# Performance work log

Hardware: AMD Instinct MI355X
Metric: run time of the kernel (lower is better)

## Reference

```python
import jax, jax.numpy as jnp
import numpy as np

D_IN, D_OUT, HEADS, D_K = 256, 256, 8, 32
B, N, L = 2, 128, 512
SCALING = 1.0 / np.sqrt(D_K)


def setup_inputs() -> dict:
    key = jax.random.key(0)
    ks = jax.random.split(key, 12)
    s = 0.02
    return {
        "query": jax.random.normal(ks[0], (B, L, D_IN), jnp.float32),
        "key": jax.random.normal(ks[1], (B, L, D_IN), jnp.float32),
        "value": jax.random.normal(ks[2], (B, N, L, D_OUT), jnp.float32),
        "mask": jax.random.uniform(ks[3], (B, 1, L, L), jnp.float32),
        "Wq": jax.random.normal(ks[4], (D_IN, HEADS * D_K), jnp.float32) * s,
        "bq": jnp.zeros((HEADS * D_K,), jnp.float32),
        "Wk": jax.random.normal(ks[5], (D_IN, HEADS * D_K), jnp.float32) * s,
        "bk": jnp.zeros((HEADS * D_K,), jnp.float32),
        "Wv": jax.random.normal(ks[6], (D_OUT, D_OUT), jnp.float32) * s,
        "bv": jnp.zeros((D_OUT,), jnp.float32),
        "Wo": jax.random.normal(ks[7], (D_OUT, D_OUT), jnp.float32) * s,
        "bo": jnp.zeros((D_OUT,), jnp.float32),
    }


def reference(query, key, value, mask, Wq, bq, Wk, bk, Wv, bv, Wo, bo):
    b, n, l = value.shape[:3]
    h, dk = HEADS, D_K
    dh = value.shape[-1] // h  # per-head value dim
    # projections -> per-head layouts
    q = (query @ Wq + bq).reshape(b, l, h, dk).transpose(0, 2, 1, 3)  # bhld
    k = (key @ Wk + bk).reshape(b, l, h, dk).transpose(0, 2, 1, 3)    # bhld
    v = (value @ Wv + bv).reshape(b, n, l, h, dh).transpose(0, 3, 1, 2, 4)  # bhnld
    q = q * SCALING
    scores = jnp.einsum('bhid,bhjd->bhij', q, k)  # (B,H,L,L)
    scores = jnp.where(mask < 0.5, jnp.finfo(scores.dtype).min, scores)
    attn = jax.nn.softmax(scores, axis=-1)
    # dropout omitted (eval mode / deterministic reference)
    out = jnp.einsum('bhij,bhnjd->bhnid', attn, v)  # (B,H,N,L,dh)
    out = out.transpose(0, 2, 3, 1, 4).reshape(b, n, l, h * dh)
    return out @ Wo + bo
```

## Files before the change

### kernel.cpp

```cpp
#include <hip/hip_runtime.h>
#include <hip/hip_bf16.h>
#include <stdint.h>

#define BB 2
#define LL 512
#define DIN 256
#define HH 8
#define DKK 32
#define NN 128
#define DM 256
#define SCALING 0.17677669529663687f

typedef unsigned short u16;
typedef float f32x4 __attribute__((ext_vector_type(4)));
typedef short s16x8 __attribute__((ext_vector_type(8)));

#define MFMA16(a, b, c) __builtin_amdgcn_mfma_f32_16x16x32_bf16((a), (b), (c), 0, 0, 0)

typedef __attribute__((address_space(3))) char lds_char;
typedef const __attribute__((address_space(1))) char glb_char;

__device__ __forceinline__ void gload16(const void* g, void* l) {
    __builtin_amdgcn_global_load_lds((glb_char*)g, (lds_char*)l, 16, 0, 0);
}

__device__ __forceinline__ u16 f2bf(float f) {
    union { float f; uint32_t i; } v; v.f = f;
    uint32_t x = v.i;
    return (u16)((x + 0x7fffu + ((x >> 16) & 1u)) >> 16);
}

__device__ __forceinline__ uint32_t pack2bf(float f0, float f1) {
    union { float f; uint32_t i; } a, b;
    a.f = f0; b.f = f1;
    return __builtin_amdgcn_perm(b.i + 0x8000u, a.i + 0x8000u, 0x07060302u);
}

__device__ __forceinline__ s16x8 ldsfrag(const u16* base, int row, int cb) {
    const char* p = (const char*)base + row * 128 + (cb ^ ((row & 7) << 4));
    return *(const s16x8*)(const void*)p;
}

__global__ __launch_bounds__(256) void prep_weights(
        const float* __restrict__ Wq, const float* __restrict__ Wk,
        const float* __restrict__ Wv, const float* __restrict__ Wo,
        u16* __restrict__ wqt, u16* __restrict__ wkt,
        u16* __restrict__ wvt, u16* __restrict__ wot) {
    int idx = blockIdx.x * 256 + threadIdx.x;
    int which = idx >> 16;
    const float* src = (which == 0) ? Wq : (which == 1) ? Wk : (which == 2) ? Wv : Wo;
    u16* dst = (which == 0) ? wqt : (which == 1) ? wkt : (which == 2) ? wvt : wot;
    int i = idx & 65535;
    int c = i & 255;
    int k = i >> 8;
    dst[(size_t)c * 256 + k] = f2bf(src[(size_t)k * 256 + c]);
}

__global__ __launch_bounds__(256) void qk_proj(
        const float* __restrict__ q_in, const float* __restrict__ k_in,
        const u16* __restrict__ wqt, const float* __restrict__ bq,
        const u16* __restrict__ wkt, const float* __restrict__ bk,
        u16* __restrict__ q_ws, u16* __restrict__ k_ws) {
    int bid = blockIdx.x;
    int isK = bid & 1;
    int r0 = (bid >> 1) * 64;
    const float* src = isK ? k_in : q_in;
    const u16* wt    = isK ? wkt : wqt;
    const float* bias = isK ? bk : bq;
    u16* dst = isK ? k_ws : q_ws;
    float scale = isK ? 1.0f : SCALING;

    int t = threadIdx.x, w = t >> 6, l = t & 63, lr = l & 15, lg = l >> 4;

    f32x4 zero = {0.f, 0.f, 0.f, 0.f};
    f32x4 acc[4][4];
#pragma unroll
    for (int m = 0; m < 4; m++)
#pragma unroll
        for (int cf = 0; cf < 4; cf++) acc[m][cf] = zero;

#pragma unroll
    for (int ks = 0; ks < 8; ks++) {
        s16x8 afr[4];
#pragma unroll
        for (int m = 0; m < 4; m++) {
            const float* p = src + (size_t)(r0 + m * 16 + lr) * DIN + ks * 32 + lg * 8;
            float4 v0 = *(const float4*)p;
            float4 v1 = *(const float4*)(p + 4);
            union { u16 u[8]; s16x8 v; } tmp;
            tmp.u[0] = f2bf(v0.x); tmp.u[1] = f2bf(v0.y);
            tmp.u[2] = f2bf(v0.z); tmp.u[3] = f2bf(v0.w);
            tmp.u[4] = f2bf(v1.x); tmp.u[5] = f2bf(v1.y);
            tmp.u[6] = f2bf(v1.z); tmp.u[7] = f2bf(v1.w);
            afr[m] = tmp.v;
        }
        s16x8 bfrg[4];
#pragma unroll
        for (int cf = 0; cf < 4; cf++)
            bfrg[cf] = *(const s16x8*)(const void*)(wt + (size_t)(w * 64 + cf * 16 + lr) * 256 + ks * 32 + lg * 8);
#pragma unroll
        for (int m = 0; m < 4; m++)
#pragma unroll
            for (int cf = 0; cf < 4; cf++) acc[m][cf] = MFMA16(afr[m], bfrg[cf], acc[m][cf]);
    }

#pragma unroll
    for (int m = 0; m < 4; m++)
#pragma unroll
        for (int cf = 0; cf < 4; cf++) {
            int c = w * 64 + cf * 16 + lr;
            int h = c >> 5, dd = c & 31;
            float bv_ = bias[c];
#pragma unroll
            for (int r = 0; r < 4; r++) {
                int row = r0 + m * 16 + 4 * lg + r;
                int b = row >> 9, li = row & 511;
                dst[(((size_t)(b * HH + h)) * LL + li) * DKK + dd] = f2bf((acc[m][cf][r] + bv_) * scale);
            }
        }
}

__global__ __launch_bounds__(256) void scores_softmax(
        const u16* __restrict__ q_ws, const u16* __restrict__ k_ws,
        const float* __restrict__ mask, u16* __restrict__ attn) {
    int bid = blockIdx.x;
    int it = bid & 15;
    int bh = bid >> 4;
    int b = bh >> 3;
    int i0 = it * 32;

    __shared__ u16 kl[LL][40];
    __shared__ u16 ql[32][40];
    __shared__ float redmx[2][32];
    __shared__ float redsm[2][32];

    int t = threadIdx.x;
    const u16* kbase = k_ws + (size_t)bh * LL * DKK;
#pragma unroll
    for (int x = 0; x < 8; x++) {
        int idx = x * 256 + t;
        int row = idx >> 2, ch = idx & 3;
        *(s16x8*)(void*)(&kl[row][ch * 8]) = *(const s16x8*)(const void*)(kbase + (size_t)row * DKK + ch * 8);
    }
    if (t < 128) {
        const u16* qbase = q_ws + (size_t)bh * LL * DKK + (size_t)i0 * DKK;
        int row = t >> 2, ch = t & 3;
        *(s16x8*)(void*)(&ql[row][ch * 8]) = *(const s16x8*)(const void*)(qbase + (size_t)row * DKK + ch * 8);
    }
    __syncthreads();

    int w = t >> 6, l = t & 63, lr = l & 15, lg = l >> 4;
    int ih = (w & 1) * 16;
    int jh = (w >> 1) * 256;
    int jhalf = w >> 1;

    s16x8 af = *(const s16x8*)(const void*)(&ql[ih + lr][lg * 8]);
    f32x4 zero = {0.f, 0.f, 0.f, 0.f};
    f32x4 acc[16];
#pragma unroll
    for (int cf = 0; cf < 16; cf++) {
        s16x8 bf = *(const s16x8*)(const void*)(&kl[jh + cf * 16 + lr][lg * 8]);
        acc[cf] = MFMA16(af, bf, zero);
    }

    const float* mrow = mask + (size_t)b * LL * LL;
    float attv[16][4];
    float mx[4], sm[4];
#pragma unroll
    for (int r = 0; r < 4; r++) mx[r] = -3.0e38f;
#pragma unroll
    for (int cf = 0; cf < 16; cf++) {
#pragma unroll
        for (int r = 0; r < 4; r++) {
            int irow = i0 + ih + 4 * lg + r;
            int jcol = jh + cf * 16 + lr;
            float mv = mrow[(size_t)irow * LL + jcol];
            float s = (mv < 0.5f) ? -1.0e30f : acc[cf][r];
            attv[cf][r] = s;
            mx[r] = fmaxf(mx[r], s);
        }
    }
#pragma unroll
    for (int d = 1; d < 16; d <<= 1)
#pragma unroll
        for (int r = 0; r < 4; r++) mx[r] = fmaxf(mx[r], __shfl_xor(mx[r], d));
#pragma unroll
    for (int r = 0; r < 4; r++) sm[r] = 0.f;
#pragma unroll
    for (int cf = 0; cf < 16; cf++)
#pragma unroll
        for (int r = 0; r < 4; r++) {
            float p = __expf(attv[cf][r] - mx[r]);
            attv[cf][r] = p;
            sm[r] += p;
        }
#pragma unroll
    for (int d = 1; d < 16; d <<= 1)
#pragma unroll
        for (int r = 0; r < 4; r++) sm[r] += __shfl_xor(sm[r], d);

    if (lr == 0) {
#pragma unroll
        for (int r = 0; r < 4; r++) {
            redmx[jhalf][ih + 4 * lg + r] = mx[r];
            redsm[jhalf][ih + 4 * lg + r] = sm[r];
        }
    }
    __syncthreads();
    float inv[4];
#pragma unroll
    for (int r = 0; r < 4; r++) {
        int row = ih + 4 * lg + r;
        float m0 = redmx[0][row], m1 = redmx[1][row];
        float s0 = redsm[0][row], s1 = redsm[1][row];
        float gm = fmaxf(m0, m1);
        float gs = s0 * __expf(m0 - gm) + s1 * __expf(m1 - gm);
        inv[r] = __expf(mx[r] - gm) / gs;
    }

    u16* abase = attn + (size_t)bh * LL * LL;
#pragma unroll
    for (int cf = 0; cf < 16; cf++)
#pragma unroll
        for (int r = 0; r < 4; r++) {
            int irow = i0 + ih + 4 * lg + r;
            int jcol = jh + cf * 16 + lr;
            abase[(size_t)irow * LL + jcol] = f2bf(attv[cf][r] * inv[r]);
        }
}

__global__ __launch_bounds__(256, 2) void vproj_gemm(
        const float* __restrict__ value, const float* __restrict__ bv,
        const u16* __restrict__ wvt, u16* __restrict__ ut) {
    __shared__ __align__(16) u16 sm[2 * 16384];

    int t = threadIdx.x;
    int nb = gridDim.x;
    int cpx = nb >> 3;
    int swz = (blockIdx.x & 7) * cpx + (blockIdx.x >> 3);
    int ct = swz & 1;
    int jt = (swz >> 1) & 3;
    int bn = swz >> 3;
    int c0 = ct * 128, j0 = jt * 128;

    int w = t >> 6, l = t & 63, lr = l & 15, lg = l >> 4;
    int wr = w >> 1, wc = w & 1;

    const float* vbase = value + ((size_t)bn * LL + j0) * DM;

    int srow = t >> 3;
    int sgc = t & 7;
    f32x4 zero = {0.f, 0.f, 0.f, 0.f};
    f32x4 acc[4][4];
#pragma unroll
    for (int m = 0; m < 4; m++)
#pragma unroll
        for (int nf = 0; nf < 4; nf++) acc[m][nf] = zero;

    auto stageA = [&](int buf, int kk) {
#pragma unroll
        for (int x = 0; x < 4; x++) {
            int row = x * 32 + srow;
            int gs = sgc ^ (row & 7);
            gload16(wvt + (size_t)(c0 + row) * 256 + kk * 64 + gs * 8,
                    (char*)&sm[buf * 16384] + (x * 256 + t) * 16);
        }
    };
    float4 breg[2][4][2];
    auto loadB = [&](int set, int kk) {
#pragma unroll
        for (int x = 0; x < 4; x++) {
            int row = x * 32 + srow;
            const float* p = vbase + (size_t)row * DM + kk * 64 + sgc * 8;
            breg[set][x][0] = *(const float4*)p;
            breg[set][x][1] = *(const float4*)(p + 4);
        }
    };
    auto writeB = [&](int buf, int set) {
#pragma unroll
        for (int x = 0; x < 4; x++) {
            int row = x * 32 + srow;
            uint32_t p0 = pack2bf(breg[set][x][0].x, breg[set][x][0].y);
            uint32_t p1 = pack2bf(breg[set][x][0].z, breg[set][x][0].w);
            uint32_t p2 = pack2bf(breg[set][x][1].x, breg[set][x][1].y);
            uint32_t p3 = pack2bf(breg[set][x][1].z, breg[set][x][1].w);
            uint32_t* dst = (uint32_t*)((char*)&sm[buf * 16384 + 8192]
                            + row * 128 + ((sgc * 16) ^ ((row & 7) << 4)));
            dst[0] = p0; dst[1] = p1; dst[2] = p2; dst[3] = p3;
        }
    };

    stageA(0, 0);
    loadB(0, 0);
    loadB(1, 1);
    writeB(0, 0);
    __syncthreads();
    int cur = 0;
#pragma unroll
    for (int kk = 0; kk < 4; kk++) {
        if (kk < 3) stageA(cur ^ 1, kk + 1);
        if (kk < 2) loadB(kk & 1, kk + 2);
        const u16* Ab = &sm[cur * 16384];
        const u16* Bb = &sm[cur * 16384 + 8192];
        s16x8 af[4][2], bf[4][2];
#pragma unroll
        for (int m = 0; m < 4; m++)
#pragma unroll
            for (int ks = 0; ks < 2; ks++)
                af[m][ks] = ldsfrag(Ab, wr * 64 + m * 16 + lr, ks * 64 + lg * 16);
#pragma unroll
        for (int nf = 0; nf < 4; nf++)
#pragma unroll
            for (int ks = 0; ks < 2; ks++)
                bf[nf][ks] = ldsfrag(Bb, wc * 64 + nf * 16 + lr, ks * 64 + lg * 16);
#pragma unroll
        for (int ks = 0; ks < 2; ks++)
#pragma unroll
            for (int m = 0; m < 4; m++)
#pragma unroll
                for (int nf = 0; nf < 4; nf++)
                    acc[m][nf] = MFMA16(af[m][ks], bf[nf][ks], acc[m][nf]);
        if (kk < 3) writeB(cur ^ 1, (kk + 1) & 1);
        __syncthreads();
        cur ^= 1;
    }

    u16* ubase = ut + (size_t)bn * DM * LL;
#pragma unroll
    for (int m = 0; m < 4; m++) {
#pragma unroll
        for (int rr = 0; rr < 4; rr++) {
            int c = c0 + wr * 64 + m * 16 + 4 * lg + rr;
            float bvv = bv[c];
#pragma unroll
            for (int nf = 0; nf < 4; nf++) {
                int j = j0 + wc * 64 + nf * 16 + lr;
                ubase[(size_t)c * LL + j] = f2bf(acc[m][nf][rr] + bvv);
            }
        }
    }
}

__global__ __launch_bounds__(256, 2) void pv_gemm(
        const u16* __restrict__ attn, const u16* __restrict__ ut,
        u16* __restrict__ Tm, int n0, int nTiles, int Nc) {
    __shared__ __align__(16) u16 sm[2 * 16384];

    int t = threadIdx.x;
    int nb = gridDim.x;
    int cpx = nb >> 3;
    int swz = (blockIdx.x & 7) * cpx + (blockIdx.x >> 3);
    int nct = swz % nTiles;
    int tmp2 = swz / nTiles;
    int it = tmp2 & 3;
    int bh = tmp2 >> 2;
    int b = bh >> 3, h = bh & 7;
    int i0 = it * 128;

    int w = t >> 6, l = t & 63, lr = l & 15, lg = l >> 4;
    int wr = w >> 1, wc = w & 1;

    const u16* arow0 = attn + (size_t)bh * LL * LL + (size_t)i0 * LL;

    f32x4 zero = {0.f, 0.f, 0.f, 0.f};
    f32x4 acc[4][4];
#pragma unroll
    for (int m = 0; m < 4; m++)
#pragma unroll
        for (int nf = 0; nf < 4; nf++) acc[m][nf] = zero;

    auto stage = [&](int buf, int kk) {
#pragma unroll
        for (int x = 0; x < 4; x++) {
            int G = x * 256 + t;
            int row = G >> 3, gc = G & 7;
            int gs = gc ^ (row & 7);
            gload16(arow0 + (size_t)row * LL + kk * 64 + gs * 8,
                    (char*)&sm[buf * 16384] + G * 16);
        }
#pragma unroll
        for (int x = 0; x < 4; x++) {
            int G = x * 256 + t;
            int row = G >> 3, gc = G & 7;
            int gs = gc ^ (row & 7);
            int nc = nct * 128 + row;
            const u16* src = ut + (((size_t)(b * NN + n0 + (nc >> 5))) * DM + h * DKK + (nc & 31)) * LL
                             + kk * 64 + gs * 8;
            gload16(src, (char*)&sm[buf * 16384 + 8192] + G * 16);
        }
    };

    stage(0, 0);
    __syncthreads();
    int cur = 0;
    for (int kk = 0; kk < 8; kk++) {
        if (kk < 7) stage(cur ^ 1, kk + 1);
        const u16* Ab = &sm[cur * 16384];
        const u16* Bb = &sm[cur * 16384 + 8192];
        s16x8 af[4][2], bf[4][2];
#pragma unroll
        for (int m = 0; m < 4; m++)
#pragma unroll
            for (int ks = 0; ks < 2; ks++)
                af[m][ks] = ldsfrag(Ab, wr * 64 + m * 16 + lr, ks * 64 + lg * 16);
#pragma unroll
        for (int nf = 0; nf < 4; nf++)
#pragma unroll
            for (int ks = 0; ks < 2; ks++)
                bf[nf][ks] = ldsfrag(Bb, wc * 64 + nf * 16 + lr, ks * 64 + lg * 16);
#pragma unroll
        for (int ks = 0; ks < 2; ks++)
#pragma unroll
            for (int m = 0; m < 4; m++)
#pragma unroll
                for (int nf = 0; nf < 4; nf++)
                    acc[m][nf] = MFMA16(af[m][ks], bf[nf][ks], acc[m][nf]);
        __syncthreads();
        cur ^= 1;
    }

#pragma unroll
    for (int m = 0; m < 4; m++) {
        int i = i0 + wr * 64 + m * 16 + 4 * lg;
#pragma unroll
        for (int nf = 0; nf < 4; nf++) {
            int nc = nct * 128 + wc * 64 + nf * 16 + lr;
            int nl = nc >> 5, cl = nc & 31;
            u16* dst = Tm + (((size_t)(b * Nc + nl)) * LL + i) * DM + h * DKK + cl;
#pragma unroll
            for (int rr = 0; rr < 4; rr++)
                dst[(size_t)rr * DM] = f2bf(acc[m][nf][rr]);
        }
    }
}

__global__ __launch_bounds__(256, 2) void wo_gemm(
        const u16* __restrict__ Tm, const u16* __restrict__ wot,
        const float* __restrict__ bo, float* __restrict__ out,
        int n0, int Nc, int nshift) {
    __shared__ __align__(16) u16 sm[2 * 16384];

    int t = threadIdx.x;
    int nb = gridDim.x;
    int cpx = nb >> 3;
    int swz = (blockIdx.x & 7) * cpx + (blockIdx.x >> 3);
    int oc = swz & 1;
    int mt = swz >> 1;
    int r0 = mt * 128;

    int w = t >> 6, l = t & 63, lr = l & 15, lg = l >> 4;
    int wr = w >> 1, wc = w & 1;

    f32x4 zero = {0.f, 0.f, 0.f, 0.f};
    f32x4 acc[4][4];
#pragma unroll
    for (int m = 0; m < 4; m++)
#pragma unroll
        for (int nf = 0; nf < 4; nf++) acc[m][nf] = zero;

    auto stage = [&](int buf, int kk) {
#pragma unroll
        for (int x = 0; x < 4; x++) {
            int G = x * 256 + t;
            int row = G >> 3, gc = G & 7;
            int gs = gc ^ (row & 7);
            gload16(Tm + (size_t)(r0 + row) * DM + kk * 64 + gs * 8,
                    (char*)&sm[buf * 16384] + G * 16);
        }
#pragma unroll
        for (int x = 0; x < 4; x++) {
            int G = x * 256 + t;
            int row = G >> 3, gc = G & 7;
            int gs = gc ^ (row & 7);
            gload16(wot + (size_t)(oc * 128 + row) * DM + kk * 64 + gs * 8,
                    (char*)&sm[buf * 16384 + 8192] + G * 16);
        }
    };

    stage(0, 0);
    __syncthreads();
    int cur = 0;
    for (int kk = 0; kk < 4; kk++) {
        if (kk < 3) stage(cur ^ 1, kk + 1);
        const u16* Ab = &sm[cur * 16384];
        const u16* Bb = &sm[cur * 16384 + 8192];
        s16x8 af[4][2], bf[4][2];
#pragma unroll
        for (int m = 0; m < 4; m++)
#pragma unroll
            for (int ks = 0; ks < 2; ks++)
                af[m][ks] = ldsfrag(Ab, wr * 64 + m * 16 + lr, ks * 64 + lg * 16);
#pragma unroll
        for (int nf = 0; nf < 4; nf++)
#pragma unroll
            for (int ks = 0; ks < 2; ks++)
                bf[nf][ks] = ldsfrag(Bb, wc * 64 + nf * 16 + lr, ks * 64 + lg * 16);
#pragma unroll
        for (int ks = 0; ks < 2; ks++)
#pragma unroll
            for (int m = 0; m < 4; m++)
#pragma unroll
                for (int nf = 0; nf < 4; nf++)
                    acc[m][nf] = MFMA16(af[m][ks], bf[nf][ks], acc[m][nf]);
        __syncthreads();
        cur ^= 1;
    }

#pragma unroll
    for (int nf = 0; nf < 4; nf++) {
        int ocol = oc * 128 + wc * 64 + nf * 16 + lr;
        float bov = bo[ocol];
#pragma unroll
        for (int m = 0; m < 4; m++) {
            int rbase = r0 + wr * 64 + m * 16 + 4 * lg;
#pragma unroll
            for (int rr = 0; rr < 4; rr++) {
                int r = rbase + rr;
                int bnl = r >> 9, i = r & 511;
                int b = bnl >> nshift, nl = bnl & (Nc - 1);
                out[(((size_t)(b * NN + n0 + nl)) * LL + i) * DM + ocol] = acc[m][nf][rr] + bov;
            }
        }
    }
}

extern "C" void kernel_launch(void* const* d_in, const int* in_sizes, int n_in,
                              void* d_out, int out_size, void* d_ws, size_t ws_size,
                              hipStream_t stream) {
    const float* query = (const float*)d_in[0];
    const float* key_  = (const float*)d_in[1];
    const float* value = (const float*)d_in[2];
    const float* mask  = (const float*)d_in[3];
    const float* Wq = (const float*)d_in[4];
    const float* bq = (const float*)d_in[5];
    const float* Wk = (const float*)d_in[6];
    const float* bk = (const float*)d_in[7];
    const float* Wv = (const float*)d_in[8];
    const float* bv = (const float*)d_in[9];
    const float* Wo = (const float*)d_in[10];
    const float* bo = (const float*)d_in[11];

    char* ws = (char*)d_ws;
    u16* wvt  = (u16*)(ws + 0);
    u16* wot  = (u16*)(ws + 131072);
    u16* qw   = (u16*)(ws + 262144);
    u16* kw   = (u16*)(ws + 786432);
    u16* attn = (u16*)(ws + 1310720);
    u16* wqt  = (u16*)(ws + 1310720);
    u16* wkt  = (u16*)(ws + 1310720 + 131072);
    u16* ut   = (u16*)(ws + 9699328);
    u16* Tm   = (u16*)(ws + 76808192);
    float* out = (float*)d_out;

    size_t avail = (ws_size > 76808192u) ? (ws_size - 76808192u) : 0;
    int Nc = 128;
    while (Nc > 4 && (size_t)Nc * 524288u > avail) Nc >>= 1;
    int nshift = 0;
    while ((1 << nshift) < Nc) nshift++;

    hipLaunchKernelGGL(prep_weights,   dim3(1024), dim3(256), 0, stream, Wq, Wk, Wv, Wo, wqt, wkt, wvt, wot);
    hipLaunchKernelGGL(qk_proj,        dim3(32),   dim3(256), 0, stream, query, key_, wqt, bq, wkt, bk, qw, kw);
    hipLaunchKernelGGL(scores_softmax, dim3(256),  dim3(256), 0, stream, qw, kw, mask, attn);
    hipLaunchKernelGGL(vproj_gemm,     dim3(2048), dim3(256), 0, stream, value, bv, wvt, ut);

    int nTiles = Nc >> 2;
    for (int n0 = 0; n0 < NN; n0 += Nc) {
        hipLaunchKernelGGL(pv_gemm, dim3(16 * 4 * nTiles), dim3(256), 0, stream,
                           attn, ut, Tm, n0, nTiles, Nc);
        hipLaunchKernelGGL(wo_gemm, dim3((BB * Nc * LL / 128) * 2), dim3(256), 0, stream,
                           Tm, wot, bo, out, n0, Nc, nshift);
    }
}
```

Before: 185.0 us.

## Make GEMM kernels persistent over multiple tiles with cross-tile prefetch

The V-projection, PV and Wo GEMM kernels now launch at most 512 blocks, and each block loops over several consecutive output tiles. The first k-slice of the next tile is staged into shared memory while the last k-slice of the current tile is being computed, so the pipeline does not drain between tiles. This aims to cut block launch and prologue costs and keep the loads flowing. In exchange there is less block-level parallelism, a longer serial chain per block, and the epilogue stores now sit inside the main loop.

```diff
diff --git a/kernel.cpp b/kernel.cpp
--- a/kernel.cpp
+++ b/kernel.cpp
@@ -231,25 +231,28 @@
 
 __global__ __launch_bounds__(256, 2) void vproj_gemm(
         const float* __restrict__ value, const float* __restrict__ bv,
-        const u16* __restrict__ wvt, u16* __restrict__ ut) {
+        const u16* __restrict__ wvt, u16* __restrict__ ut, int tpb) {
     __shared__ __align__(16) u16 sm[2 * 16384];
 
     int t = threadIdx.x;
     int nb = gridDim.x;
     int cpx = nb >> 3;
-    int swz = (blockIdx.x & 7) * cpx + (blockIdx.x >> 3);
-    int ct = swz & 1;
-    int jt = (swz >> 1) & 3;
-    int bn = swz >> 3;
-    int c0 = ct * 128, j0 = jt * 128;
+    int sb = (blockIdx.x & 7) * cpx + (blockIdx.x >> 3);
+    int g0 = sb * tpb;
 
     int w = t >> 6, l = t & 63, lr = l & 15, lg = l >> 4;
     int wr = w >> 1, wc = w & 1;
-
-    const float* vbase = value + ((size_t)bn * LL + j0) * DM;
-
     int srow = t >> 3;
     int sgc = t & 7;
+
+    int c0_c, j0_c, bn_c, c0_n, j0_n, bn_n;
+    const float *vb_c, *vb_n;
+    {
+        int ct = g0 & 1, jt = (g0 >> 1) & 3, bn = g0 >> 3;
+        c0_c = ct * 128; j0_c = jt * 128; bn_c = bn;
+        vb_c = value + ((size_t)bn * LL + j0_c) * DM;
+    }
+
     f32x4 zero = {0.f, 0.f, 0.f, 0.f};
     f32x4 acc[4][4];
 #pragma unroll
@@ -257,7 +260,7 @@
 #pragma unroll
         for (int nf = 0; nf < 4; nf++) acc[m][nf] = zero;
 
-    auto stageA = [&](int buf, int kk) {
+    auto stageA = [&](int buf, int c0, int kk) {
 #pragma unroll
         for (int x = 0; x < 4; x++) {
             int row = x * 32 + srow;
@@ -267,11 +270,11 @@
         }
     };
     float4 breg[2][4][2];
-    auto loadB = [&](int set, int kk) {
+    auto loadB = [&](int set, const float* vb, int kk) {
 #pragma unroll
         for (int x = 0; x < 4; x++) {
             int row = x * 32 + srow;
-            const float* p = vbase + (size_t)row * DM + kk * 64 + sgc * 8;
+            const float* p = vb + (size_t)row * DM + kk * 64 + sgc * 8;
             breg[set][x][0] = *(const float4*)p;
             breg[set][x][1] = *(const float4*)(p + 4);
         }
@@ -290,77 +293,100 @@
         }
     };
 
-    stageA(0, 0);
-    loadB(0, 0);
-    loadB(1, 1);
+    stageA(0, c0_c, 0);
+    loadB(0, vb_c, 0);
+    loadB(1, vb_c, 1);
     writeB(0, 0);
     __syncthreads();
     int cur = 0;
-#pragma unroll
-    for (int kk = 0; kk < 4; kk++) {
-        if (kk < 3) stageA(cur ^ 1, kk + 1);
-        if (kk < 2) loadB(kk & 1, kk + 2);
-        const u16* Ab = &sm[cur * 16384];
-        const u16* Bb = &sm[cur * 16384 + 8192];
-        s16x8 af[4][2], bf[4][2];
-#pragma unroll
-        for (int m = 0; m < 4; m++)
+
+    for (int tt = 0; tt < tpb; tt++) {
+        int gn = (tt + 1 < tpb) ? (g0 + tt + 1) : g0;
+        {
+            int ct = gn & 1, jt = (gn >> 1) & 3, bn = gn >> 3;
+            c0_n = ct * 128; j0_n = jt * 128; bn_n = bn;
+            vb_n = value + ((size_t)bn * LL + j0_n) * DM;
+        }
+#pragma unroll
+        for (int kk = 0; kk < 4; kk++) {
+            if (kk < 3) stageA(cur ^ 1, c0_c, kk + 1);
+            else        stageA(cur ^ 1, c0_n, 0);
+            if (kk < 2) loadB(kk & 1, vb_c, kk + 2);
+            else        loadB(kk & 1, vb_n, kk - 2);
+            const u16* Ab = &sm[cur * 16384];
+            const u16* Bb = &sm[cur * 16384 + 8192];
+            s16x8 af[4][2], bf[4][2];
+#pragma unroll
+            for (int m = 0; m < 4; m++)
+#pragma unroll
+                for (int ks = 0; ks < 2; ks++)
+                    af[m][ks] = ldsfrag(Ab, wr * 64 + m * 16 + lr, ks * 64 + lg * 16);
+#pragma unroll
+            for (int nf = 0; nf < 4; nf++)
+#pragma unroll
+                for (int ks = 0; ks < 2; ks++)
+                    bf[nf][ks] = ldsfrag(Bb, wc * 64 + nf * 16 + lr, ks * 64 + lg * 16);
 #pragma unroll
             for (int ks = 0; ks < 2; ks++)
-                af[m][ks] = ldsfrag(Ab, wr * 64 + m * 16 + lr, ks * 64 + lg * 16);
-#pragma unroll
-        for (int nf = 0; nf < 4; nf++)
-#pragma unroll
-            for (int ks = 0; ks < 2; ks++)
-                bf[nf][ks] = ldsfrag(Bb, wc * 64 + nf * 16 + lr, ks * 64 + lg * 16);
-#pragma unroll
-        for (int ks = 0; ks < 2; ks++)
-#pragma unroll
-            for (int m = 0; m < 4; m++)
-#pragma unroll
-                for (int nf = 0; nf < 4; nf++)
-                    acc[m][nf] = MFMA16(af[m][ks], bf[nf][ks], acc[m][nf]);
-        if (kk < 3) writeB(cur ^ 1, (kk + 1) & 1);
-        __syncthreads();
-        cur ^= 1;
-    }
-
-    u16* ubase = ut + (size_t)bn * DM * LL;
-#pragma unroll
-    for (int m = 0; m < 4; m++) {
-#pragma unroll
-        for (int rr = 0; rr < 4; rr++) {
-            int c = c0 + wr * 64 + m * 16 + 4 * lg + rr;
-            float bvv = bv[c];
-#pragma unroll
-            for (int nf = 0; nf < 4; nf++) {
-                int j = j0 + wc * 64 + nf * 16 + lr;
-                ubase[(size_t)c * LL + j] = f2bf(acc[m][nf][rr] + bvv);
+#pragma unroll
+                for (int m = 0; m < 4; m++)
+#pragma unroll
+                    for (int nf = 0; nf < 4; nf++)
+                        acc[m][nf] = MFMA16(af[m][ks], bf[nf][ks], acc[m][nf]);
+            writeB(cur ^ 1, (kk + 1) & 1);
+            if (kk == 3) {
+                u16* ubase = ut + (size_t)bn_c * DM * LL;
+#pragma unroll
+                for (int m = 0; m < 4; m++) {
+#pragma unroll
+                    for (int rr = 0; rr < 4; rr++) {
+                        int c = c0_c + wr * 64 + m * 16 + 4 * lg + rr;
+                        float bvv = bv[c];
+#pragma unroll
+                        for (int nf = 0; nf < 4; nf++) {
+                            int j = j0_c + wc * 64 + nf * 16 + lr;
+                            ubase[(size_t)c * LL + j] = f2bf(acc[m][nf][rr] + bvv);
+                        }
+                    }
+                }
+#pragma unroll
+                for (int m = 0; m < 4; m++)
+#pragma unroll
+                    for (int nf = 0; nf < 4; nf++) acc[m][nf] = zero;
             }
-        }
+            __syncthreads();
+            cur ^= 1;
+        }
+        c0_c = c0_n; j0_c = j0_n; bn_c = bn_n; vb_c = vb_n;
     }
 }
 
 __global__ __launch_bounds__(256, 2) void pv_gemm(
         const u16* __restrict__ attn, const u16* __restrict__ ut,
-        u16* __restrict__ Tm, int n0, int nTiles, int Nc) {
+        u16* __restrict__ Tm, int n0, int nTiles, int Nc, int tpb) {
     __shared__ __align__(16) u16 sm[2 * 16384];
 
     int t = threadIdx.x;
     int nb = gridDim.x;
     int cpx = nb >> 3;
-    int swz = (blockIdx.x & 7) * cpx + (blockIdx.x >> 3);
-    int nct = swz % nTiles;
-    int tmp2 = swz / nTiles;
-    int it = tmp2 & 3;
-    int bh = tmp2 >> 2;
-    int b = bh >> 3, h = bh & 7;
-    int i0 = it * 128;
+    int sb = (blockIdx.x & 7) * cpx + (blockIdx.x >> 3);
+    int g0 = sb * tpb;
 
     int w = t >> 6, l = t & 63, lr = l & 15, lg = l >> 4;
     int wr = w >> 1, wc = w & 1;
 
-    const u16* arow0 = attn + (size_t)bh * LL * LL + (size_t)i0 * LL;
+    int nct_c, b_c, h_c, i0_c, nct_n;
+    const u16 *aB_c, *aB_n;
+    const u16 *uB_c, *uB_n;
+    {
+        int g = g0;
+        nct_c = g % nTiles;
+        int tmp = g / nTiles;
+        int it = tmp & 3, bh = tmp >> 2;
+        b_c = bh >> 3; h_c = bh & 7; i0_c = it * 128;
+        aB_c = attn + (size_t)bh * LL * LL + (size_t)i0_c * LL;
+        uB_c = ut + ((size_t)((b_c * NN + n0) * DM + h_c * DKK)) * LL;
+    }
 
     f32x4 zero = {0.f, 0.f, 0.f, 0.f};
     f32x4 acc[4][4];
@@ -369,13 +395,13 @@
 #pragma unroll
         for (int nf = 0; nf < 4; nf++) acc[m][nf] = zero;
 
-    auto stage = [&](int buf, int kk) {
+    auto stage = [&](int buf, const u16* aB, const u16* uB, int nct, int kk) {
 #pragma unroll
         for (int x = 0; x < 4; x++) {
             int G = x * 256 + t;
             int row = G >> 3, gc = G & 7;
             int gs = gc ^ (row & 7);
-            gload16(arow0 + (size_t)row * LL + kk * 64 + gs * 8,
+            gload16(aB + (size_t)row * LL + kk * 64 + gs * 8,
                     (char*)&sm[buf * 16384] + G * 16);
         }
 #pragma unroll
@@ -383,53 +409,78 @@
             int G = x * 256 + t;
             int row = G >> 3, gc = G & 7;
             int gs = gc ^ (row & 7);
-            int nc = nct * 128 + row;
-            const u16* src = ut + (((size_t)(b * NN + n0 + (nc >> 5))) * DM + h * DKK + (nc & 31)) * LL
+            const u16* src = uB + ((size_t)((nct * 4 + (row >> 5)) * DM + (row & 31))) * LL
                              + kk * 64 + gs * 8;
             gload16(src, (char*)&sm[buf * 16384 + 8192] + G * 16);
         }
     };
 
-    stage(0, 0);
+    stage(0, aB_c, uB_c, nct_c, 0);
     __syncthreads();
     int cur = 0;
-    for (int kk = 0; kk < 8; kk++) {
-        if (kk < 7) stage(cur ^ 1, kk + 1);
-        const u16* Ab = &sm[cur * 16384];
-        const u16* Bb = &sm[cur * 16384 + 8192];
-        s16x8 af[4][2], bf[4][2];
-#pragma unroll
-        for (int m = 0; m < 4; m++)
+
+    for (int tt = 0; tt < tpb; tt++) {
+        int gn = (tt + 1 < tpb) ? (g0 + tt + 1) : g0;
+        {
+            nct_n = gn % nTiles;
+            int tmp = gn / nTiles;
+            int it = tmp & 3, bh = tmp >> 2;
+            int bb = bh >> 3, hh = bh & 7;
+            aB_n = attn + (size_t)bh * LL * LL + (size_t)(it * 128) * LL;
+            uB_n = ut + ((size_t)((bb * NN + n0) * DM + hh * DKK)) * LL;
+        }
+#pragma unroll
+        for (int kk = 0; kk < 8; kk++) {
+            if (kk < 7) stage(cur ^ 1, aB_c, uB_c, nct_c, kk + 1);
+            else        stage(cur ^ 1, aB_n, uB_n, nct_n, 0);
+            const u16* Ab = &sm[cur * 16384];
+            const u16* Bb = &sm[cur * 16384 + 8192];
+            s16x8 af[4][2], bf[4][2];
+#pragma unroll
+            for (int m = 0; m < 4; m++)
+#pragma unroll
+                for (int ks = 0; ks < 2; ks++)
+                    af[m][ks] = ldsfrag(Ab, wr * 64 + m * 16 + lr, ks * 64 + lg * 16);
+#pragma unroll
+            for (int nf = 0; nf < 4; nf++)
+#pragma unroll
+                for (int ks = 0; ks < 2; ks++)
+                    bf[nf][ks] = ldsfrag(Bb, wc * 64 + nf * 16 + lr, ks * 64 + lg * 16);
 #pragma unroll
             for (int ks = 0; ks < 2; ks++)
-                af[m][ks] = ldsfrag(Ab, wr * 64 + m * 16 + lr, ks * 64 + lg * 16);
-#pragma unroll
-        for (int nf = 0; nf < 4; nf++)
-#pragma unroll
-            for (int ks = 0; ks < 2; ks++)
-                bf[nf][ks] = ldsfrag(Bb, wc * 64 + nf * 16 + lr, ks * 64 + lg * 16);
-#pragma unroll
-        for (int ks = 0; ks < 2; ks++)
-#pragma unroll
-            for (int m = 0; m < 4; m++)
-#pragma unroll
-                for (int nf = 0; nf < 4; nf++)
-                    acc[m][nf] = MFMA16(af[m][ks], bf[nf][ks], acc[m][nf]);
-        __syncthreads();
-        cur ^= 1;
-    }
-
-#pragma unroll
-    for (int m = 0; m < 4; m++) {
-        int i = i0 + wr * 64 + m * 16 + 4 * lg;
-#pragma unroll
-        for (int nf = 0; nf < 4; nf++) {
-            int nc = nct * 128 + wc * 64 + nf * 16 + lr;
-            int nl = nc >> 5, cl = nc & 31;
-            u16* dst = Tm + (((size_t)(b * Nc + nl)) * LL + i) * DM + h * DKK + cl;
-#pragma unroll
-            for (int rr = 0; rr < 4; rr++)
-                dst[(size_t)rr * DM] = f2bf(acc[m][nf][rr]);
+#pragma unroll
+                for (int m = 0; m < 4; m++)
+#pragma unroll
+                    for (int nf = 0; nf < 4; nf++)
+                        acc[m][nf] = MFMA16(af[m][ks], bf[nf][ks], acc[m][nf]);
+            if (kk == 7) {
+#pragma unroll
+                for (int m = 0; m < 4; m++) {
+                    int i = i0_c + wr * 64 + m * 16 + 4 * lg;
+#pragma unroll
+                    for (int nf = 0; nf < 4; nf++) {
+                        int nc = nct_c * 128 + wc * 64 + nf * 16 + lr;
+                        int nl = nc >> 5, cl = nc & 31;
+                        u16* dst = Tm + (((size_t)(b_c * Nc + nl)) * LL + i) * DM + h_c * DKK + cl;
+#pragma unroll
+                        for (int rr = 0; rr < 4; rr++)
+                            dst[(size_t)rr * DM] = f2bf(acc[m][nf][rr]);
+                    }
+                }
+#pragma unroll
+                for (int m = 0; m < 4; m++)
+#pragma unroll
+                    for (int nf = 0; nf < 4; nf++) acc[m][nf] = zero;
+            }
+            __syncthreads();
+            cur ^= 1;
+        }
+        nct_c = nct_n; aB_c = aB_n; uB_c = uB_n;
+        {
+            int g = (tt + 1 < tpb) ? (g0 + tt + 1) : g0;
+            int tmp = g / nTiles;
+            int it = tmp & 3, bh = tmp >> 2;
+            b_c = bh >> 3; h_c = bh & 7; i0_c = it * 128;
         }
     }
 }
@@ -437,20 +488,21 @@
 __global__ __launch_bounds__(256, 2) void wo_gemm(
         const u16* __restrict__ Tm, const u16* __restrict__ wot,
         const float* __restrict__ bo, float* __restrict__ out,
-        int n0, int Nc, int nshift) {
+        int n0, int Nc, int nshift, int tpb) {
     __shared__ __align__(16) u16 sm[2 * 16384];
 
     int t = threadIdx.x;
     int nb = gridDim.x;
     int cpx = nb >> 3;
-    int swz = (blockIdx.x & 7) * cpx + (blockIdx.x >> 3);
-    int oc = swz & 1;
-    int mt = swz >> 1;
-    int r0 = mt * 128;
+    int sb = (blockIdx.x & 7) * cpx + (blockIdx.x >> 3);
+    int g0 = sb * tpb;
 
     int w = t >> 6, l = t & 63, lr = l & 15, lg = l >> 4;
     int wr = w >> 1, wc = w & 1;
 
+    int oc_c, r0_c, oc_n, r0_n;
+    { int g = g0; oc_c = g & 1; r0_c = (g >> 1) * 128; }
+
     f32x4 zero = {0.f, 0.f, 0.f, 0.f};
     f32x4 acc[4][4];
 #pragma unroll
@@ -458,7 +510,7 @@
 #pragma unroll
         for (int nf = 0; nf < 4; nf++) acc[m][nf] = zero;
 
-    auto stage = [&](int buf, int kk) {
+    auto stage = [&](int buf, int r0, int oc, int kk) {
 #pragma unroll
         for (int x = 0; x < 4; x++) {
             int G = x * 256 + t;
@@ -477,50 +529,63 @@
         }
     };
 
-    stage(0, 0);
+    stage(0, r0_c, oc_c, 0);
     __syncthreads();
     int cur = 0;
-    for (int kk = 0; kk < 4; kk++) {
-        if (kk < 3) stage(cur ^ 1, kk + 1);
-        const u16* Ab = &sm[cur * 16384];
-        const u16* Bb = &sm[cur * 16384 + 8192];
-        s16x8 af[4][2], bf[4][2];
-#pragma unroll
-        for (int m = 0; m < 4; m++)
+
+    for (int tt = 0; tt < tpb; tt++) {
+        int gn = (tt + 1 < tpb) ? (g0 + tt + 1) : g0;
+        oc_n = gn & 1; r0_n = (gn >> 1) * 128;
+#pragma unroll
+        for (int kk = 0; kk < 4; kk++) {
+            if (kk < 3) stage(cur ^ 1, r0_c, oc_c, kk + 1);
+            else        stage(cur ^ 1, r0_n, oc_n, 0);
+            const u16* Ab = &sm[cur * 16384];
+            const u16* Bb = &sm[cur * 16384 + 8192];
+            s16x8 af[4][2], bf[4][2];
+#pragma unroll
+            for (int m = 0; m < 4; m++)
+#pragma unroll
+                for (int ks = 0; ks < 2; ks++)
+                    af[m][ks] = ldsfrag(Ab, wr * 64 + m * 16 + lr, ks * 64 + lg * 16);
+#pragma unroll
+            for (int nf = 0; nf < 4; nf++)
+#pragma unroll
+                for (int ks = 0; ks < 2; ks++)
+                    bf[nf][ks] = ldsfrag(Bb, wc * 64 + nf * 16 + lr, ks * 64 + lg * 16);
 #pragma unroll
             for (int ks = 0; ks < 2; ks++)
-                af[m][ks] = ldsfrag(Ab, wr * 64 + m * 16 + lr, ks * 64 + lg * 16);
-#pragma unroll
-        for (int nf = 0; nf < 4; nf++)
-#pragma unroll
-            for (int ks = 0; ks < 2; ks++)
-                bf[nf][ks] = ldsfrag(Bb, wc * 64 + nf * 16 + lr, ks * 64 + lg * 16);
-#pragma unroll
-        for (int ks = 0; ks < 2; ks++)
-#pragma unroll
-            for (int m = 0; m < 4; m++)
-#pragma unroll
-                for (int nf = 0; nf < 4; nf++)
-                    acc[m][nf] = MFMA16(af[m][ks], bf[nf][ks], acc[m][nf]);
-        __syncthreads();
-        cur ^= 1;
-    }
-
-#pragma unroll
-    for (int nf = 0; nf < 4; nf++) {
-        int ocol = oc * 128 + wc * 64 + nf * 16 + lr;
-        float bov = bo[ocol];
-#pragma unroll
-        for (int m = 0; m < 4; m++) {
-            int rbase = r0 + wr * 64 + m * 16 + 4 * lg;
-#pragma unroll
-            for (int rr = 0; rr < 4; rr++) {
-                int r = rbase + rr;
-                int bnl = r >> 9, i = r & 511;
-                int b = bnl >> nshift, nl = bnl & (Nc - 1);
-                out[(((size_t)(b * NN + n0 + nl)) * LL + i) * DM + ocol] = acc[m][nf][rr] + bov;
+#pragma unroll
+                for (int m = 0; m < 4; m++)
+#pragma unroll
+                    for (int nf = 0; nf < 4; nf++)
+                        acc[m][nf] = MFMA16(af[m][ks], bf[nf][ks], acc[m][nf]);
+            if (kk == 3) {
+#pragma unroll
+                for (int nf = 0; nf < 4; nf++) {
+                    int ocol = oc_c * 128 + wc * 64 + nf * 16 + lr;
+                    float bov = bo[ocol];
+#pragma unroll
+                    for (int m = 0; m < 4; m++) {
+                        int rbase = r0_c + wr * 64 + m * 16 + 4 * lg;
+#pragma unroll
+                        for (int rr = 0; rr < 4; rr++) {
+                            int r = rbase + rr;
+                            int bnl = r >> 9, i = r & 511;
+                            int b = bnl >> nshift, nl = bnl & (Nc - 1);
+                            out[(((size_t)(b * NN + n0 + nl)) * LL + i) * DM + ocol] = acc[m][nf][rr] + bov;
+                        }
+                    }
+                }
+#pragma unroll
+                for (int m = 0; m < 4; m++)
+#pragma unroll
+                    for (int nf = 0; nf < 4; nf++) acc[m][nf] = zero;
             }
-        }
+            __syncthreads();
+            cur ^= 1;
+        }
+        oc_c = oc_n; r0_c = r0_n;
     }
 }
 
@@ -561,13 +626,20 @@
     hipLaunchKernelGGL(prep_weights,   dim3(1024), dim3(256), 0, stream, Wq, Wk, Wv, Wo, wqt, wkt, wvt, wot);
     hipLaunchKernelGGL(qk_proj,        dim3(32),   dim3(256), 0, stream, query, key_, wqt, bq, wkt, bk, qw, kw);
     hipLaunchKernelGGL(scores_softmax, dim3(256),  dim3(256), 0, stream, qw, kw, mask, attn);
-    hipLaunchKernelGGL(vproj_gemm,     dim3(2048), dim3(256), 0, stream, value, bv, wvt, ut);
+
+    hipLaunchKernelGGL(vproj_gemm,     dim3(512),  dim3(256), 0, stream, value, bv, wvt, ut, 4);
 
     int nTiles = Nc >> 2;
+    int totP = 16 * 4 * nTiles;
+    int nbP = (totP < 512) ? totP : 512;
+    int tpbP = totP / nbP;
+    int totW = (BB * Nc * LL / 128) * 2;
+    int nbW = (totW < 512) ? totW : 512;
+    int tpbW = totW / nbW;
     for (int n0 = 0; n0 < NN; n0 += Nc) {
-        hipLaunchKernelGGL(pv_gemm, dim3(16 * 4 * nTiles), dim3(256), 0, stream,
-                           attn, ut, Tm, n0, nTiles, Nc);
-        hipLaunchKernelGGL(wo_gemm, dim3((BB * Nc * LL / 128) * 2), dim3(256), 0, stream,
-                           Tm, wot, bo, out, n0, Nc, nshift);
-    }
-}
+        hipLaunchKernelGGL(pv_gemm, dim3(nbP), dim3(256), 0, stream,
+                           attn, ut, Tm, n0, nTiles, Nc, tpbP);
+        hipLaunchKernelGGL(wo_gemm, dim3(nbW), dim3(256), 0, stream,
+                           Tm, wot, bo, out, n0, Nc, nshift, tpbW);
+    }
+}
```

New measurement: 209.2 us. 13.1% more time.
